# Optimization experiments

Measured on AMD Instinct MI355X. Metric: run time of the kernel, lower is better.

The kernel has to match this reference:

```python
import jax, jax.numpy as jnp
import numpy as np

N = 3072      # nodes
D = 256       # embed_dim
H = 8         # heads
E = 98304     # edges (avg degree 32)
B = 16        # graphs in batch


def setup_inputs() -> dict:
    key = jax.random.key(0)
    ks = jax.random.split(key, 14)
    w = lambda k, sh: jax.random.normal(k, sh, jnp.float32) * 0.02
    return {
        "x": jax.random.normal(ks[0], (N, D), jnp.float32),
        "edge_attr": jax.random.normal(ks[1], (E, 4), jnp.float32),
        "Wq": w(ks[2], (D, D)), "bq": jnp.zeros((D,), jnp.float32),
        "Wk": w(ks[3], (D, D)), "bk": jnp.zeros((D,), jnp.float32),
        "Wv": w(ks[4], (D, D)), "bv": jnp.zeros((D,), jnp.float32),
        "Wo": w(ks[5], (D, D)), "bo": jnp.zeros((D,), jnp.float32),
        "We": w(ks[6], (4, H)), "be": jnp.zeros((H,), jnp.float32),
        "edge_index": jax.random.randint(ks[7], (2, E), 0, N),
        "batch": jnp.sort(jax.random.randint(ks[8], (N,), 0, B)),
    }


def reference(x, edge_attr, Wq, bq, Wk, bk, Wv, bv, Wo, bo, We, be,
              edge_index, batch):
    n, d = x.shape
    h = be.shape[0]
    hd = d // h
    # projections -> [h, n, hd]
    Q = (x @ Wq + bq).reshape(n, h, hd).transpose(1, 0, 2)
    K = (x @ Wk + bk).reshape(n, h, hd).transpose(1, 0, 2)
    V = (x @ Wv + bv).reshape(n, h, hd).transpose(1, 0, 2)
    # dense attention scores [h, n, n]
    scores = jnp.einsum('hnd,hmd->hnm', Q, K) / np.float32(np.sqrt(hd))
    # per-edge bias scatter-add (accumulate over duplicate edges)
    edge_bias = edge_attr @ We + be                     # [E, h]
    scores = scores.at[:, edge_index[0], edge_index[1]].add(edge_bias.T)
    # block-diagonal batch mask
    same_graph = batch[:, None] == batch[None, :]       # [n, n]
    scores = jnp.where(same_graph[None], scores, -jnp.inf)
    attn = jax.nn.softmax(scores, axis=-1)              # dropout: eval mode (identity)
    out = jnp.einsum('hnm,hmd->hnd', attn, V)           # [h, n, hd]
    out = out.transpose(1, 0, 2).reshape(n, d)
    return out @ Wo + bo
```

## Files before the change

kernel.cpp:

```cpp
#include <hip/hip_runtime.h>
#include <hip/hip_bf16.h>
#include <math.h>

#define N_NODES 3072
#define NPAD    3104
#define DIM     256
#define NH      8
#define HD      32
#define E_EDGES 98304
#define B_GRAPHS 16
#define RCAP    96
#define MAXC    332
#define TR      16
#define SCALE   0.17677669529663689f

typedef __attribute__((ext_vector_type(8))) short bf16x8;
typedef __attribute__((ext_vector_type(4))) float f32x4;
typedef __attribute__((ext_vector_type(4))) unsigned short ushort4v;

__device__ inline unsigned short f2b(float f) {
    __hip_bfloat16 h = __float2bfloat16(f);
    return *reinterpret_cast<unsigned short*>(&h);
}
__device__ inline float b2f(unsigned short u) {
    __hip_bfloat16 h = *reinterpret_cast<__hip_bfloat16*>(&u);
    return __bfloat162float(h);
}


__device__ inline void xsplit_body(int u, int t, const float* __restrict__ x,
                                   unsigned short* __restrict__ xh,
                                   unsigned short* __restrict__ xl) {
    const int gid = u * 256 + t;
    float4 v = ((const float4*)x)[gid];
    ushort4v h, l;
    float c[4] = {v.x, v.y, v.z, v.w};
    #pragma unroll
    for (int i = 0; i < 4; ++i) {
        unsigned short hi = f2b(c[i]);
        h[i] = hi;
        l[i] = f2b(c[i] - b2f(hi));
    }
    ((ushort4v*)xh)[gid] = h;
    ((ushort4v*)xl)[gid] = l;
}

__device__ inline void wtrans_body(int wb, int t,
                                   const float* __restrict__ Wq, const float* __restrict__ Wk,
                                   const float* __restrict__ Wv, const float* __restrict__ Wo,
                                   unsigned short* __restrict__ Wth,
                                   unsigned short* __restrict__ Wtl,
                                   float (*tile)[33]) {
    const int mat = wb >> 6, tidx = wb & 63;
    const int tk = (tidx >> 3) * 32, tn = (tidx & 7) * 32;
    const float* W = (mat == 0) ? Wq : (mat == 1) ? Wk : (mat == 2) ? Wv : Wo;
    const int kk = t >> 5, nn = t & 31;
    #pragma unroll
    for (int p = 0; p < 4; ++p)
        tile[nn][kk + p * 8] = W[(size_t)(tk + kk + p * 8) * DIM + tn + nn];
    __syncthreads();
    const int n = t >> 3, kq = (t & 7) * 4;
    ushort4v h, l;
    #pragma unroll
    for (int i = 0; i < 4; ++i) {
        float v = tile[n][kq + i];
        unsigned short hi = f2b(v);
        h[i] = hi;
        l[i] = f2b(v - b2f(hi));
    }
    size_t o = (size_t)mat * DIM * DIM + (size_t)(tn + n) * DIM + tk + kq;
    *(ushort4v*)(Wth + o) = h;
    *(ushort4v*)(Wtl + o) = l;
}

__device__ inline void vtpad_body(int i, const int* __restrict__ batch,
                                  unsigned short* __restrict__ VT,
                                  int* __restrict__ gstart) {
    VT[(size_t)(i >> 5) * NPAD + N_NODES + (i & 31)] = 0;
    if (i < N_NODES) {
        int bb = batch[i];
        int bp = (i == 0) ? -1 : batch[i - 1];
        for (int g = bp + 1; g <= bb; ++g) gstart[g] = i;
        if (i == N_NODES - 1)
            for (int g = bb + 1; g <= B_GRAPHS; ++g) gstart[g] = N_NODES;
    }
}

__device__ inline void edge_body(int e, const float* __restrict__ ea,
                                 const float* __restrict__ We, const float* __restrict__ be,
                                 const int* __restrict__ erow, const int* __restrict__ ecolin,
                                 float* __restrict__ ebias, int* __restrict__ tcur,
                                 unsigned int* __restrict__ tbuck) {
    const int row = erow[e];
    const int col = ecolin[e];
    int pos = atomicAdd(&tcur[row], 1);
    if (pos < RCAP)
        tbuck[(size_t)row * RCAP + pos] = ((unsigned int)e << 12) | (unsigned int)col;
    float4 a = ((const float4*)ea)[e];
    #pragma unroll
    for (int h = 0; h < NH; ++h) {
        float bb = fmaf(a.x, We[0 * NH + h],
                   fmaf(a.y, We[1 * NH + h],
                   fmaf(a.z, We[2 * NH + h],
                   fmaf(a.w, We[3 * NH + h], be[h]))));
        ebias[(size_t)h * E_EDGES + e] = bb;
    }
}

__device__ inline void qkv_body(int u, int t,
                                const unsigned short* __restrict__ xh, const unsigned short* __restrict__ xl,
                                const unsigned short* __restrict__ Wth, const unsigned short* __restrict__ Wtl,
                                const float* __restrict__ bq, const float* __restrict__ bk,
                                const float* __restrict__ bv,
                                unsigned short* __restrict__ Qb, unsigned short* __restrict__ Kb,
                                unsigned short* __restrict__ VT) {
    const int w = t >> 6, lane = t & 63;
    const int l16 = lane & 15, lq = lane >> 4;
    const int bx = u % 96, by = u / 96;
    const int mat = by >> 2;
    const int rb = bx * 32 + (w & 1) * 16;
    const int nb = (by & 3) * 64 + (w >> 1) * 32;
    const unsigned short* Wh = Wth + (size_t)mat * DIM * DIM;
    const unsigned short* Wl = Wtl + (size_t)mat * DIM * DIM;

    f32x4 acc[2] = {{0,0,0,0},{0,0,0,0}};

    if (mat < 2) {
        const size_t arow = (size_t)(rb + l16) * DIM + (lq << 3);
        #pragma unroll
        for (int kc = 0; kc < 8; ++kc) {
            const int k = kc * 32;
            bf16x8 ah = *(const bf16x8*)(xh + arow + k);
            bf16x8 al = *(const bf16x8*)(xl + arow + k);
            #pragma unroll
            for (int ct = 0; ct < 2; ++ct) {
                const size_t bo_ = (size_t)(nb + ct * 16 + l16) * DIM + k + (lq << 3);
                bf16x8 bh = *(const bf16x8*)(Wh + bo_);
                bf16x8 bl = *(const bf16x8*)(Wl + bo_);
                acc[ct] = __builtin_amdgcn_mfma_f32_16x16x32_bf16(ah, bh, acc[ct], 0, 0, 0);
                acc[ct] = __builtin_amdgcn_mfma_f32_16x16x32_bf16(ah, bl, acc[ct], 0, 0, 0);
                acc[ct] = __builtin_amdgcn_mfma_f32_16x16x32_bf16(al, bh, acc[ct], 0, 0, 0);
            }
        }
        const float* bias = (mat == 0) ? bq : bk;
        unsigned short* outp = (mat == 0) ? Qb : Kb;
        #pragma unroll
        for (int ct = 0; ct < 2; ++ct) {
            const int n = nb + ct * 16 + l16;
            const float bvl = bias[n];
            #pragma unroll
            for (int r = 0; r < 4; ++r)
                outp[(size_t)(rb + lq * 4 + r) * DIM + n] = f2b(acc[ct][r] + bvl);
        }
    } else {
        const size_t brow = (size_t)(rb + l16) * DIM + (lq << 3);
        #pragma unroll
        for (int kc = 0; kc < 8; ++kc) {
            const int k = kc * 32;
            bf16x8 bxh = *(const bf16x8*)(xh + brow + k);
            bf16x8 bxl = *(const bf16x8*)(xl + brow + k);
            #pragma unroll
            for (int ct = 0; ct < 2; ++ct) {
                const size_t ao_ = (size_t)(nb + ct * 16 + l16) * DIM + k + (lq << 3);
                bf16x8 awh = *(const bf16x8*)(Wh + ao_);
                bf16x8 awl = *(const bf16x8*)(Wl + ao_);
                acc[ct] = __builtin_amdgcn_mfma_f32_16x16x32_bf16(awh, bxh, acc[ct], 0, 0, 0);
                acc[ct] = __builtin_amdgcn_mfma_f32_16x16x32_bf16(awh, bxl, acc[ct], 0, 0, 0);
                acc[ct] = __builtin_amdgcn_mfma_f32_16x16x32_bf16(awl, bxh, acc[ct], 0, 0, 0);
            }
        }
        #pragma unroll
        for (int ct = 0; ct < 2; ++ct) {
            #pragma unroll
            for (int r = 0; r < 4; ++r) {
                const int ncol = nb + ct * 16 + lq * 4 + r;
                VT[(size_t)ncol * NPAD + rb + l16] = f2b(acc[ct][r] + bv[ncol]);
            }
        }
    }
}

__device__ inline void attn_body(int g, int tile_, int h, int t,
                                 const unsigned short* __restrict__ Qb,
                                 const unsigned short* __restrict__ Kb,
                                 const unsigned short* __restrict__ VT,
                                 const int* __restrict__ gstart,
                                 const int* __restrict__ tcur,
                                 const unsigned int* __restrict__ tbuck,
                                 const float* __restrict__ ebias,
                                 unsigned short* __restrict__ preh,
                                 unsigned short* __restrict__ prel,
                                 float (*s)[MAXC], float* rowinv) {
    const int gs = gstart[g], ge = gstart[g + 1];
    const int row0 = gs + tile_ * TR;
    if (row0 >= ge) return;
    const int nrows = min(TR, ge - row0);
    const int ncols = ge - gs;
    const int ags   = gs & ~15;
    const int coff  = gs - ags;
    const int tcols = coff + ncols;
    const int cpad  = (tcols + 31) & ~31;
    const int wave = t >> 6, lane = t & 63;
    const int l16 = lane & 15, lq = lane >> 4;

    {
        int arow = min(row0 + l16, N_NODES - 1);
        const bf16x8 aq = *(const bf16x8*)(Qb + (size_t)arow * DIM + h * HD + (lq << 3));
        const int nchunk16 = (tcols + 15) >> 4;
        for (int j = wave; j < nchunk16; j += 4) {
            const int c0 = j << 4;
            int krow = min(ags + c0 + l16, N_NODES - 1);
            bf16x8 bk = *(const bf16x8*)(Kb + (size_t)krow * DIM + h * HD + (lq << 3));
            f32x4 d = {0.f, 0.f, 0.f, 0.f};
            d = __builtin_amdgcn_mfma_f32_16x16x32_bf16(aq, bk, d, 0, 0, 0);
            const int col = c0 + l16, rbase = lq * 4;
            #pragma unroll
            for (int r = 0; r < 4; ++r) s[rbase + r][col] = d[r] * SCALE;
        }
    }
    __syncthreads();

    {
        const int r = t >> 4, sub = t & 15;
        if (r < nrows) {
            const int cnt = min(tcur[row0 + r], RCAP);
            const unsigned int* bk = tbuck + (size_t)(row0 + r) * RCAP;
            for (int idx = sub; idx < cnt; idx += 16) {
                unsigned int p = bk[idx];
                int c = (int)(p & 0xFFFu) - gs;
                if (c >= 0 && c < ncols)
                    atomicAdd(&s[r][coff + c], ebias[(size_t)h * E_EDGES + (p >> 12)]);
            }
        }
    }
    __syncthreads();

    {
        const int r = t >> 4, sub = t & 15;
        if (r < nrows) {
            float m = -INFINITY;
            for (int c = coff + sub; c < tcols; c += 16) m = fmaxf(m, s[r][c]);
            m = fmaxf(m, __shfl_xor(m, 1, 16));
            m = fmaxf(m, __shfl_xor(m, 2, 16));
            m = fmaxf(m, __shfl_xor(m, 4, 16));
            m = fmaxf(m, __shfl_xor(m, 8, 16));
            float sum = 0.f;
            for (int c = sub; c < cpad; c += 16) {
                float e = 0.f;
                if (c >= coff && c < tcols) e = __expf(s[r][c] - m);
                sum += e;
                s[r][c] = e;
            }
            sum += __shfl_xor(sum, 1, 16);
            sum += __shfl_xor(sum, 2, 16);
            sum += __shfl_xor(sum, 4, 16);
            sum += __shfl_xor(sum, 8, 16);
            if (sub == 0) rowinv[r] = 1.0f / sum;
        } else {
            for (int c = sub; c < cpad; c += 16) s[r][c] = 0.f;
        }
    }
    __syncthreads();

    f32x4 o = {0.f, 0.f, 0.f, 0.f};
    {
        const int half = wave >> 1, par = wave & 1;
        const int kout = l16 + (half << 4);
        const int nchunk32 = cpad >> 5;
        const unsigned short* vrow = VT + (size_t)(h * HD + kout) * NPAD + ags + (lq << 3);
        for (int j = par; j < nchunk32; j += 2) {
            const int c0 = j << 5;
            const float4 p0 = *(const float4*)&s[l16][c0 + (lq << 3)];
            const float4 p1 = *(const float4*)&s[l16][c0 + (lq << 3) + 4];
            bf16x8 ap;
            ap[0] = f2b(p0.x); ap[1] = f2b(p0.y); ap[2] = f2b(p0.z); ap[3] = f2b(p0.w);
            ap[4] = f2b(p1.x); ap[5] = f2b(p1.y); ap[6] = f2b(p1.z); ap[7] = f2b(p1.w);
            bf16x8 bv = *(const bf16x8*)(vrow + c0);
            o = __builtin_amdgcn_mfma_f32_16x16x32_bf16(ap, bv, o, 0, 0, 0);
        }
    }
    __syncthreads();
    {
        float* red = &s[0][0];
        const int rbase = lq * 4;
        #pragma unroll
        for (int r = 0; r < 4; ++r)
            red[((wave << 4) + rbase + r) * 17 + l16] = o[r];
    }
    __syncthreads();
    {
        const int row = t >> 4, kl = t & 15;
        if (row < nrows) {
            float* red = &s[0][0];
            float v0 = red[(row) * 17 + kl]        + red[(16 + row) * 17 + kl];
            float v1 = red[(32 + row) * 17 + kl]   + red[(48 + row) * 17 + kl];
            float sc = rowinv[row];
            size_t ob = (size_t)(row0 + row) * DIM + h * HD;
            float f0 = v0 * sc, f1 = v1 * sc;
            unsigned short h0 = f2b(f0), h1 = f2b(f1);
            preh[ob + kl]      = h0;
            preh[ob + 16 + kl] = h1;
            prel[ob + kl]      = f2b(f0 - b2f(h0));
            prel[ob + 16 + kl] = f2b(f1 - b2f(h1));
        }
    }
}

__device__ inline void out_body(int bxo, int byo, int t,
                                const unsigned short* __restrict__ preh,
                                const unsigned short* __restrict__ prel,
                                const unsigned short* __restrict__ Wth,
                                const unsigned short* __restrict__ Wtl,
                                const float* __restrict__ bo, float* __restrict__ out) {
    const int w = t >> 6, lane = t & 63;
    const int l16 = lane & 15, lq = lane >> 4;
    const int rb = bxo * 16;
    const int nb = byo * 128 + w * 32;
    const unsigned short* Wh = Wth + (size_t)3 * DIM * DIM;
    const unsigned short* Wl = Wtl + (size_t)3 * DIM * DIM;

    f32x4 acc[2] = {{0,0,0,0},{0,0,0,0}};
    const size_t arow = (size_t)(rb + l16) * DIM + (lq << 3);

    #pragma unroll
    for (int kc = 0; kc < 8; ++kc) {
        const int k = kc * 32;
        bf16x8 ah = *(const bf16x8*)(preh + arow + k);
        bf16x8 al = *(const bf16x8*)(prel + arow + k);
        #pragma unroll
        for (int ct = 0; ct < 2; ++ct) {
            const size_t bo_ = (size_t)(nb + ct * 16 + l16) * DIM + k + (lq << 3);
            bf16x8 bh = *(const bf16x8*)(Wh + bo_);
            bf16x8 bl = *(const bf16x8*)(Wl + bo_);
            acc[ct] = __builtin_amdgcn_mfma_f32_16x16x32_bf16(ah, bh, acc[ct], 0, 0, 0);
            acc[ct] = __builtin_amdgcn_mfma_f32_16x16x32_bf16(ah, bl, acc[ct], 0, 0, 0);
            acc[ct] = __builtin_amdgcn_mfma_f32_16x16x32_bf16(al, bh, acc[ct], 0, 0, 0);
        }
    }

    #pragma unroll
    for (int ct = 0; ct < 2; ++ct) {
        const int n = nb + ct * 16 + l16;
        const float bvl = bo[n];
        #pragma unroll
        for (int r = 0; r < 4; ++r)
            out[(size_t)(rb + lq * 4 + r) * DIM + n] = acc[ct][r] + bvl;
    }
}

__global__ __launch_bounds__(256) void prep_a(
    const float* __restrict__ x,
    const float* __restrict__ Wq, const float* __restrict__ Wk,
    const float* __restrict__ Wv, const float* __restrict__ Wo,
    unsigned short* __restrict__ xh, unsigned short* __restrict__ xl,
    unsigned short* __restrict__ Wth, unsigned short* __restrict__ Wtl,
    int* __restrict__ tcur)
{
    __shared__ float tile[32][33];
    const int b = blockIdx.x, t = threadIdx.x;
    if (b < 768)        xsplit_body(b, t, x, xh, xl);
    else if (b < 1024)  wtrans_body(b - 768, t, Wq, Wk, Wv, Wo, Wth, Wtl, tile);
    else                tcur[(b - 1024) * 256 + t] = 0;
}

__global__ __launch_bounds__(256) void stage2(
    const unsigned short* __restrict__ xh, const unsigned short* __restrict__ xl,
    const unsigned short* __restrict__ Wth, const unsigned short* __restrict__ Wtl,
    const float* __restrict__ bq, const float* __restrict__ bk,
    const float* __restrict__ bv,
    const float* __restrict__ ea, const float* __restrict__ We,
    const float* __restrict__ be,
    const int* __restrict__ erow, const int* __restrict__ ecolin,
    const int* __restrict__ batch,
    unsigned short* __restrict__ Qb, unsigned short* __restrict__ Kb,
    unsigned short* __restrict__ VT,
    float* __restrict__ ebias, int* __restrict__ gstart,
    int* __restrict__ tcur, unsigned int* __restrict__ tbuck)
{
    const int b = blockIdx.x, t = threadIdx.x;
    if (b < 384)        edge_body(b * 256 + t, ea, We, be, erow, ecolin, ebias, tcur, tbuck);
    else if (b < 1536)  qkv_body(b - 384, t, xh, xl, Wth, Wtl, bq, bk, bv, Qb, Kb, VT);
    else                vtpad_body((b - 1536) * 256 + t, batch, VT, gstart);
}

__global__ __launch_bounds__(256) void attn(
    const unsigned short* __restrict__ Qb, const unsigned short* __restrict__ Kb,
    const unsigned short* __restrict__ VT,
    const int* __restrict__ gstart,
    const int* __restrict__ tcur, const unsigned int* __restrict__ tbuck,
    const float* __restrict__ ebias,
    unsigned short* __restrict__ preh, unsigned short* __restrict__ prel)
{
    __shared__ __align__(16) float s[TR][MAXC];
    __shared__ float rowinv[TR];
    attn_body(blockIdx.x, blockIdx.y, blockIdx.z, threadIdx.x,
              Qb, Kb, VT, gstart, tcur, tbuck, ebias, preh, prel, s, rowinv);
}

__global__ __launch_bounds__(256) void out_mfma(
    const unsigned short* __restrict__ preh, const unsigned short* __restrict__ prel,
    const unsigned short* __restrict__ Wth, const unsigned short* __restrict__ Wtl,
    const float* __restrict__ bo, float* __restrict__ out)
{
    out_body(blockIdx.x, blockIdx.y, threadIdx.x, preh, prel, Wth, Wtl, bo, out);
}

extern "C" void kernel_launch(void* const* d_in, const int* in_sizes, int n_in,
                              void* d_out, int out_size, void* d_ws, size_t ws_size,
                              hipStream_t stream) {
    const float* x   = (const float*)d_in[0];
    const float* ea  = (const float*)d_in[1];
    const float* Wq  = (const float*)d_in[2];  const float* bq = (const float*)d_in[3];
    const float* Wk  = (const float*)d_in[4];  const float* bk = (const float*)d_in[5];
    const float* Wv  = (const float*)d_in[6];  const float* bv = (const float*)d_in[7];
    const float* Wo  = (const float*)d_in[8];  const float* bo = (const float*)d_in[9];
    const float* We  = (const float*)d_in[10]; const float* be = (const float*)d_in[11];
    const int*   eidx  = (const int*)d_in[12];
    const int*   batch = (const int*)d_in[13];
    const int* erow   = eidx;
    const int* ecolin = eidx + E_EDGES;

    const size_t ND = (size_t)N_NODES * DIM;
    const size_t WD = (size_t)DIM * DIM;

    unsigned short* Qb   = (unsigned short*)d_ws;
    unsigned short* Kb   = Qb + ND;
    unsigned short* VT   = Kb + ND;
    unsigned short* preh = VT + (size_t)DIM * NPAD;
    unsigned short* prel = preh + ND;
    unsigned short* xh   = prel + ND;
    unsigned short* xl   = xh + ND;
    unsigned short* Wth  = xl + ND;
    unsigned short* Wtl  = Wth + 4 * WD;
    unsigned int* tbuck  = (unsigned int*)(Wtl + 4 * WD);
    float* ebias  = (float*)(tbuck + (size_t)N_NODES * RCAP);
    int* tcur     = (int*)(ebias + (size_t)NH * E_EDGES);
    int* gstart   = tcur + N_NODES;

    prep_a<<<dim3(1036), dim3(256), 0, stream>>>(x, Wq, Wk, Wv, Wo,
                                                 xh, xl, Wth, Wtl, tcur);
    stage2<<<dim3(1568), dim3(256), 0, stream>>>(xh, xl, Wth, Wtl, bq, bk, bv,
                                                 ea, We, be, erow, ecolin, batch,
                                                 Qb, Kb, VT, ebias, gstart, tcur, tbuck);
    attn<<<dim3(B_GRAPHS, 24, NH), dim3(256), 0, stream>>>(Qb, Kb, VT, gstart,
                                                           tcur, tbuck, ebias, preh, prel);
    out_mfma<<<dim3(192, 2), dim3(256), 0, stream>>>(preh, prel, Wth, Wtl, bo, (float*)d_out);
}
```

Before: 154.6 us.

## Fuse four launches into one persistent kernel with grid-wide barriers

Replaces the four separate kernel launches with a single persistent kernel of 1024 blocks. The blocks loop over the work units of each stage and synchronise between stages with atomic-counter global barriers, and a memset resets the barrier memory. The vtpad work moves into the first stage. The aim is to remove launch gaps and inter-kernel drain overhead, at the cost of spin-barrier latency, a co-residency requirement that is assumed via launch bounds of 4 blocks per CU, and a timeout break in the spin loop that could silently produce wrong results.

```diff
diff --git a/kernel.cpp b/kernel.cpp
--- a/kernel.cpp
+++ b/kernel.cpp
@@ -13,6 +13,7 @@
 #define MAXC    332
 #define TR      16
 #define SCALE   0.17677669529663689f
+#define NBLK    1024
 
 typedef __attribute__((ext_vector_type(8))) short bf16x8;
 typedef __attribute__((ext_vector_type(4))) float f32x4;
@@ -25,6 +26,27 @@
 __device__ inline float b2f(unsigned short u) {
     __hip_bfloat16 h = *reinterpret_cast<__hip_bfloat16*>(&u);
     return __bfloat162float(h);
+}
+
+__device__ inline void gbarrier(unsigned* slot) {
+    __syncthreads();
+    if (threadIdx.x == 0) {
+        __threadfence();
+        unsigned a = __hip_atomic_fetch_add(&slot[0], 1u, __ATOMIC_RELAXED,
+                                            __HIP_MEMORY_SCOPE_AGENT);
+        if (a + 1u == (unsigned)NBLK) {
+            __hip_atomic_store(&slot[1], 1u, __ATOMIC_RELEASE, __HIP_MEMORY_SCOPE_AGENT);
+        } else {
+            long spins = 0;
+            while (__hip_atomic_load(&slot[1], __ATOMIC_RELAXED,
+                                     __HIP_MEMORY_SCOPE_AGENT) == 0u) {
+                __builtin_amdgcn_s_sleep(32);
+                if (++spins > (1L << 21)) break;
+            }
+        }
+        __threadfence();
+    }
+    __syncthreads();
 }
 
 
@@ -348,61 +370,64 @@
     }
 }
 
-__global__ __launch_bounds__(256) void prep_a(
+__global__ __launch_bounds__(256, 4) void fused(
     const float* __restrict__ x,
     const float* __restrict__ Wq, const float* __restrict__ Wk,
     const float* __restrict__ Wv, const float* __restrict__ Wo,
-    unsigned short* __restrict__ xh, unsigned short* __restrict__ xl,
-    unsigned short* __restrict__ Wth, unsigned short* __restrict__ Wtl,
-    int* __restrict__ tcur)
-{
-    __shared__ float tile[32][33];
-    const int b = blockIdx.x, t = threadIdx.x;
-    if (b < 768)        xsplit_body(b, t, x, xh, xl);
-    else if (b < 1024)  wtrans_body(b - 768, t, Wq, Wk, Wv, Wo, Wth, Wtl, tile);
-    else                tcur[(b - 1024) * 256 + t] = 0;
-}
-
-__global__ __launch_bounds__(256) void stage2(
-    const unsigned short* __restrict__ xh, const unsigned short* __restrict__ xl,
-    const unsigned short* __restrict__ Wth, const unsigned short* __restrict__ Wtl,
-    const float* __restrict__ bq, const float* __restrict__ bk,
-    const float* __restrict__ bv,
     const float* __restrict__ ea, const float* __restrict__ We,
     const float* __restrict__ be,
     const int* __restrict__ erow, const int* __restrict__ ecolin,
+    const float* __restrict__ bq, const float* __restrict__ bk,
+    const float* __restrict__ bv, const float* __restrict__ bo,
     const int* __restrict__ batch,
+    unsigned short* __restrict__ xh, unsigned short* __restrict__ xl,
+    unsigned short* __restrict__ Wth, unsigned short* __restrict__ Wtl,
     unsigned short* __restrict__ Qb, unsigned short* __restrict__ Kb,
-    unsigned short* __restrict__ VT,
+    unsigned short* __restrict__ VT, unsigned short* __restrict__ preh,
+    unsigned short* __restrict__ prel,
     float* __restrict__ ebias, int* __restrict__ gstart,
-    int* __restrict__ tcur, unsigned int* __restrict__ tbuck)
+    int* __restrict__ tcur, unsigned int* __restrict__ tbuck,
+    unsigned* __restrict__ barmem,
+    float* __restrict__ out)
 {
-    const int b = blockIdx.x, t = threadIdx.x;
-    if (b < 384)        edge_body(b * 256 + t, ea, We, be, erow, ecolin, ebias, tcur, tbuck);
-    else if (b < 1536)  qkv_body(b - 384, t, xh, xl, Wth, Wtl, bq, bk, bv, Qb, Kb, VT);
-    else                vtpad_body((b - 1536) * 256 + t, batch, VT, gstart);
-}
-
-__global__ __launch_bounds__(256) void attn(
-    const unsigned short* __restrict__ Qb, const unsigned short* __restrict__ Kb,
-    const unsigned short* __restrict__ VT,
-    const int* __restrict__ gstart,
-    const int* __restrict__ tcur, const unsigned int* __restrict__ tbuck,
-    const float* __restrict__ ebias,
-    unsigned short* __restrict__ preh, unsigned short* __restrict__ prel)
-{
-    __shared__ __align__(16) float s[TR][MAXC];
-    __shared__ float rowinv[TR];
-    attn_body(blockIdx.x, blockIdx.y, blockIdx.z, threadIdx.x,
-              Qb, Kb, VT, gstart, tcur, tbuck, ebias, preh, prel, s, rowinv);
-}
-
-__global__ __launch_bounds__(256) void out_mfma(
-    const unsigned short* __restrict__ preh, const unsigned short* __restrict__ prel,
-    const unsigned short* __restrict__ Wth, const unsigned short* __restrict__ Wtl,
-    const float* __restrict__ bo, float* __restrict__ out)
-{
-    out_body(blockIdx.x, blockIdx.y, threadIdx.x, preh, prel, Wth, Wtl, bo, out);
+    __shared__ __align__(16) float smem[TR * MAXC + TR];
+    const int t = threadIdx.x;
+    const int G = gridDim.x;
+
+    for (int u = blockIdx.x; u < 1068; u += G) {
+        if (u < 768) {
+            xsplit_body(u, t, x, xh, xl);
+        } else if (u < 1024) {
+            wtrans_body(u - 768, t, Wq, Wk, Wv, Wo, Wth, Wtl, (float(*)[33])smem);
+            __syncthreads();
+        } else if (u < 1056) {
+            vtpad_body((u - 1024) * 256 + t, batch, VT, gstart);
+        } else {
+            tcur[(u - 1056) * 256 + t] = 0;
+        }
+    }
+    gbarrier(barmem + 0);
+
+    for (int u = blockIdx.x; u < 1536; u += G) {
+        if (u < 384) edge_body(u * 256 + t, ea, We, be, erow, ecolin, ebias, tcur, tbuck);
+        else         qkv_body(u - 384, t, xh, xl, Wth, Wtl, bq, bk, bv, Qb, Kb, VT);
+    }
+    gbarrier(barmem + 32);
+
+    {
+        float (*s)[MAXC] = (float(*)[MAXC])smem;
+        float* rowinv = smem + TR * MAXC;
+        for (int u = blockIdx.x; u < 3072; u += G) {
+            const int g = u & 15, r2 = u >> 4;
+            attn_body(g, r2 % 24, r2 / 24, t, Qb, Kb, VT, gstart, tcur, tbuck,
+                      ebias, preh, prel, s, rowinv);
+            __syncthreads();
+        }
+    }
+    gbarrier(barmem + 64);
+
+    for (int u = blockIdx.x; u < 384; u += G)
+        out_body(u % 192, u / 192, t, preh, prel, Wth, Wtl, bo, out);
 }
 
 extern "C" void kernel_launch(void* const* d_in, const int* in_sizes, int n_in,
@@ -436,13 +461,13 @@
     float* ebias  = (float*)(tbuck + (size_t)N_NODES * RCAP);
     int* tcur     = (int*)(ebias + (size_t)NH * E_EDGES);
     int* gstart   = tcur + N_NODES;
-
-    prep_a<<<dim3(1036), dim3(256), 0, stream>>>(x, Wq, Wk, Wv, Wo,
-                                                 xh, xl, Wth, Wtl, tcur);
-    stage2<<<dim3(1568), dim3(256), 0, stream>>>(xh, xl, Wth, Wtl, bq, bk, bv,
-                                                 ea, We, be, erow, ecolin, batch,
-                                                 Qb, Kb, VT, ebias, gstart, tcur, tbuck);
-    attn<<<dim3(B_GRAPHS, 24, NH), dim3(256), 0, stream>>>(Qb, Kb, VT, gstart,
-                                                           tcur, tbuck, ebias, preh, prel);
-    out_mfma<<<dim3(192, 2), dim3(256), 0, stream>>>(preh, prel, Wth, Wtl, bo, (float*)d_out);
-}
+    uintptr_t bp  = (uintptr_t)(gstart + B_GRAPHS + 1);
+    unsigned* barmem = (unsigned*)((bp + 127) & ~(uintptr_t)127);
+
+    hipMemsetAsync(barmem, 0, 3 * 128, stream);
+    fused<<<dim3(NBLK), dim3(256), 0, stream>>>(
+        x, Wq, Wk, Wv, Wo, ea, We, be, erow, ecolin,
+        bq, bk, bv, bo, batch,
+        xh, xl, Wth, Wtl, Qb, Kb, VT, preh, prel,
+        ebias, gstart, tcur, tbuck, barmem, (float*)d_out);
+}
```

New measurement: 490.0 us. 3.17x slower.

## Fuse attention and output projection into one kernel looping over heads

Applied to the files above, without the earlier changes.

Merges the per-head attention kernel and the output-projection kernel into a single kernel. Each block handles one 16-row tile for all 8 heads in sequence, keeping the concatenated head outputs in shared memory. It then runs the Wo MFMA projection directly, with the bf16 hi/lo split done in registers. This removes the preh/prel global round trip and one launch, but cuts grid parallelism by a factor of eight and serializes the heads within a block.

```diff
diff --git a/kernel.cpp b/kernel.cpp
--- a/kernel.cpp
+++ b/kernel.cpp
@@ -11,6 +11,7 @@
 #define B_GRAPHS 16
 #define RCAP    96
 #define MAXC    332
+#define PSTR    260
 #define TR      16
 #define SCALE   0.17677669529663689f
 
@@ -180,26 +181,17 @@
     }
 }
 
-__device__ inline void attn_body(int g, int tile_, int h, int t,
+__device__ inline void attn_head(int h, int row0, int nrows, int gs,
+                                 int ncols, int ags, int coff, int tcols, int cpad,
+                                 int t,
                                  const unsigned short* __restrict__ Qb,
                                  const unsigned short* __restrict__ Kb,
                                  const unsigned short* __restrict__ VT,
-                                 const int* __restrict__ gstart,
                                  const int* __restrict__ tcur,
                                  const unsigned int* __restrict__ tbuck,
                                  const float* __restrict__ ebias,
-                                 unsigned short* __restrict__ preh,
-                                 unsigned short* __restrict__ prel,
-                                 float (*s)[MAXC], float* rowinv) {
-    const int gs = gstart[g], ge = gstart[g + 1];
-    const int row0 = gs + tile_ * TR;
-    if (row0 >= ge) return;
-    const int nrows = min(TR, ge - row0);
-    const int ncols = ge - gs;
-    const int ags   = gs & ~15;
-    const int coff  = gs - ags;
-    const int tcols = coff + ncols;
-    const int cpad  = (tcols + 31) & ~31;
+                                 float (*s)[MAXC], float* rowinv,
+                                 float (*pre)[PSTR]) {
     const int wave = t >> 6, lane = t & 63;
     const int l16 = lane & 15, lq = lane >> 4;
 
@@ -295,56 +287,9 @@
             float v0 = red[(row) * 17 + kl]        + red[(16 + row) * 17 + kl];
             float v1 = red[(32 + row) * 17 + kl]   + red[(48 + row) * 17 + kl];
             float sc = rowinv[row];
-            size_t ob = (size_t)(row0 + row) * DIM + h * HD;
-            float f0 = v0 * sc, f1 = v1 * sc;
-            unsigned short h0 = f2b(f0), h1 = f2b(f1);
-            preh[ob + kl]      = h0;
-            preh[ob + 16 + kl] = h1;
-            prel[ob + kl]      = f2b(f0 - b2f(h0));
-            prel[ob + 16 + kl] = f2b(f1 - b2f(h1));
-        }
-    }
-}
-
-__device__ inline void out_body(int bxo, int byo, int t,
-                                const unsigned short* __restrict__ preh,
-                                const unsigned short* __restrict__ prel,
-                                const unsigned short* __restrict__ Wth,
-                                const unsigned short* __restrict__ Wtl,
-                                const float* __restrict__ bo, float* __restrict__ out) {
-    const int w = t >> 6, lane = t & 63;
-    const int l16 = lane & 15, lq = lane >> 4;
-    const int rb = bxo * 16;
-    const int nb = byo * 128 + w * 32;
-    const unsigned short* Wh = Wth + (size_t)3 * DIM * DIM;
-    const unsigned short* Wl = Wtl + (size_t)3 * DIM * DIM;
-
-    f32x4 acc[2] = {{0,0,0,0},{0,0,0,0}};
-    const size_t arow = (size_t)(rb + l16) * DIM + (lq << 3);
-
-    #pragma unroll
-    for (int kc = 0; kc < 8; ++kc) {
-        const int k = kc * 32;
-        bf16x8 ah = *(const bf16x8*)(preh + arow + k);
-        bf16x8 al = *(const bf16x8*)(prel + arow + k);
-        #pragma unroll
-        for (int ct = 0; ct < 2; ++ct) {
-            const size_t bo_ = (size_t)(nb + ct * 16 + l16) * DIM + k + (lq << 3);
-            bf16x8 bh = *(const bf16x8*)(Wh + bo_);
-            bf16x8 bl = *(const bf16x8*)(Wl + bo_);
-            acc[ct] = __builtin_amdgcn_mfma_f32_16x16x32_bf16(ah, bh, acc[ct], 0, 0, 0);
-            acc[ct] = __builtin_amdgcn_mfma_f32_16x16x32_bf16(ah, bl, acc[ct], 0, 0, 0);
-            acc[ct] = __builtin_amdgcn_mfma_f32_16x16x32_bf16(al, bh, acc[ct], 0, 0, 0);
-        }
-    }
-
-    #pragma unroll
-    for (int ct = 0; ct < 2; ++ct) {
-        const int n = nb + ct * 16 + l16;
-        const float bvl = bo[n];
-        #pragma unroll
-        for (int r = 0; r < 4; ++r)
-            out[(size_t)(rb + lq * 4 + r) * DIM + n] = acc[ct][r] + bvl;
+            pre[row][h * HD + kl]      = v0 * sc;
+            pre[row][h * HD + 16 + kl] = v1 * sc;
+        }
     }
 }
 
@@ -383,26 +328,82 @@
     else                vtpad_body((b - 1536) * 256 + t, batch, VT, gstart);
 }
 
-__global__ __launch_bounds__(256) void attn(
+__global__ __launch_bounds__(256) void attn_out(
     const unsigned short* __restrict__ Qb, const unsigned short* __restrict__ Kb,
     const unsigned short* __restrict__ VT,
     const int* __restrict__ gstart,
     const int* __restrict__ tcur, const unsigned int* __restrict__ tbuck,
     const float* __restrict__ ebias,
-    unsigned short* __restrict__ preh, unsigned short* __restrict__ prel)
-{
-    __shared__ __align__(16) float s[TR][MAXC];
-    __shared__ float rowinv[TR];
-    attn_body(blockIdx.x, blockIdx.y, blockIdx.z, threadIdx.x,
-              Qb, Kb, VT, gstart, tcur, tbuck, ebias, preh, prel, s, rowinv);
-}
-
-__global__ __launch_bounds__(256) void out_mfma(
-    const unsigned short* __restrict__ preh, const unsigned short* __restrict__ prel,
     const unsigned short* __restrict__ Wth, const unsigned short* __restrict__ Wtl,
     const float* __restrict__ bo, float* __restrict__ out)
 {
-    out_body(blockIdx.x, blockIdx.y, threadIdx.x, preh, prel, Wth, Wtl, bo, out);
+    __shared__ __align__(16) float s[TR][MAXC];
+    __shared__ __align__(16) float pre[TR][PSTR];
+    __shared__ float rowinv[TR];
+
+    const int g = blockIdx.x, tile_ = blockIdx.y;
+    const int gs = gstart[g], ge = gstart[g + 1];
+    const int row0 = gs + tile_ * TR;
+    if (row0 >= ge) return;
+    const int nrows = min(TR, ge - row0);
+    const int ncols = ge - gs;
+    const int ags   = gs & ~15;
+    const int coff  = gs - ags;
+    const int tcols = coff + ncols;
+    const int cpad  = (tcols + 31) & ~31;
+    const int t = threadIdx.x;
+
+    for (int h = 0; h < NH; ++h) {
+        attn_head(h, row0, nrows, gs, ncols, ags, coff, tcols, cpad, t,
+                  Qb, Kb, VT, tcur, tbuck, ebias, s, rowinv, pre);
+        __syncthreads();
+    }
+
+    for (int i = t; i < (TR - nrows) * 256; i += 256)
+        pre[nrows + (i >> 8)][i & 255] = 0.f;
+    __syncthreads();
+
+    const int w = t >> 6, lane = t & 63;
+    const int l16 = lane & 15, lq = lane >> 4;
+    const unsigned short* Wh = Wth + (size_t)3 * DIM * DIM;
+    const unsigned short* Wl = Wtl + (size_t)3 * DIM * DIM;
+
+    f32x4 acc[4] = {{0,0,0,0},{0,0,0,0},{0,0,0,0},{0,0,0,0}};
+    #pragma unroll
+    for (int kc = 0; kc < 8; ++kc) {
+        const int k = kc * 32;
+        const float4 a0 = *(const float4*)&pre[l16][k + (lq << 3)];
+        const float4 a1 = *(const float4*)&pre[l16][k + (lq << 3) + 4];
+        bf16x8 ah, al;
+        ah[0] = f2b(a0.x); al[0] = f2b(a0.x - b2f(ah[0]));
+        ah[1] = f2b(a0.y); al[1] = f2b(a0.y - b2f(ah[1]));
+        ah[2] = f2b(a0.z); al[2] = f2b(a0.z - b2f(ah[2]));
+        ah[3] = f2b(a0.w); al[3] = f2b(a0.w - b2f(ah[3]));
+        ah[4] = f2b(a1.x); al[4] = f2b(a1.x - b2f(ah[4]));
+        ah[5] = f2b(a1.y); al[5] = f2b(a1.y - b2f(ah[5]));
+        ah[6] = f2b(a1.z); al[6] = f2b(a1.z - b2f(ah[6]));
+        ah[7] = f2b(a1.w); al[7] = f2b(a1.w - b2f(ah[7]));
+        #pragma unroll
+        for (int ct = 0; ct < 4; ++ct) {
+            const size_t bo_ = (size_t)(w * 64 + ct * 16 + l16) * DIM + k + (lq << 3);
+            bf16x8 bh = *(const bf16x8*)(Wh + bo_);
+            bf16x8 bl = *(const bf16x8*)(Wl + bo_);
+            acc[ct] = __builtin_amdgcn_mfma_f32_16x16x32_bf16(ah, bh, acc[ct], 0, 0, 0);
+            acc[ct] = __builtin_amdgcn_mfma_f32_16x16x32_bf16(ah, bl, acc[ct], 0, 0, 0);
+            acc[ct] = __builtin_amdgcn_mfma_f32_16x16x32_bf16(al, bh, acc[ct], 0, 0, 0);
+        }
+    }
+    #pragma unroll
+    for (int ct = 0; ct < 4; ++ct) {
+        const int n = w * 64 + ct * 16 + l16;
+        const float bvl = bo[n];
+        #pragma unroll
+        for (int r = 0; r < 4; ++r) {
+            const int rr = lq * 4 + r;
+            if (rr < nrows)
+                out[(size_t)(row0 + rr) * DIM + n] = acc[ct][r] + bvl;
+        }
+    }
 }
 
 extern "C" void kernel_launch(void* const* d_in, const int* in_sizes, int n_in,
@@ -426,9 +427,7 @@
     unsigned short* Qb   = (unsigned short*)d_ws;
     unsigned short* Kb   = Qb + ND;
     unsigned short* VT   = Kb + ND;
-    unsigned short* preh = VT + (size_t)DIM * NPAD;
-    unsigned short* prel = preh + ND;
-    unsigned short* xh   = prel + ND;
+    unsigned short* xh   = VT + (size_t)DIM * NPAD;
     unsigned short* xl   = xh + ND;
     unsigned short* Wth  = xl + ND;
     unsigned short* Wtl  = Wth + 4 * WD;
@@ -442,7 +441,7 @@
     stage2<<<dim3(1568), dim3(256), 0, stream>>>(xh, xl, Wth, Wtl, bq, bk, bv,
                                                  ea, We, be, erow, ecolin, batch,
                                                  Qb, Kb, VT, ebias, gstart, tcur, tbuck);
-    attn<<<dim3(B_GRAPHS, 24, NH), dim3(256), 0, stream>>>(Qb, Kb, VT, gstart,
-                                                           tcur, tbuck, ebias, preh, prel);
-    out_mfma<<<dim3(192, 2), dim3(256), 0, stream>>>(preh, prel, Wth, Wtl, bo, (float*)d_out);
-}
+    attn_out<<<dim3(B_GRAPHS, 24), dim3(256), 0, stream>>>(Qb, Kb, VT, gstart,
+                                                           tcur, tbuck, ebias,
+                                                           Wth, Wtl, bo, (float*)d_out);
+}
```

New measurement: 184.4 us. 1.19x slower.
